# Optimization experiments

Measured on AMD Instinct MI355X. Metric: run time of the kernel, lower is better.

Reference implementation:

```python
import jax, jax.numpy as jnp
import numpy as np

EMBED_DIM = 1024
NUM_HEADS = 16
HEAD_DIM = EMBED_DIM // NUM_HEADS
B, L = 4, 2048


def setup_inputs() -> dict:
    key = jax.random.key(0)
    k1, k2, k3 = jax.random.split(key, 3)
    s = 1.0 / np.sqrt(EMBED_DIM)
    x = jax.random.normal(k1, (B, L, EMBED_DIM), dtype=jnp.float32)
    w_qkv = jax.random.normal(k2, (EMBED_DIM, 3 * EMBED_DIM), dtype=jnp.float32) * s
    b_qkv = jnp.zeros((3 * EMBED_DIM,), dtype=jnp.float32)
    w_out = jax.random.normal(k3, (EMBED_DIM, EMBED_DIM), dtype=jnp.float32) * s
    b_out = jnp.zeros((EMBED_DIM,), dtype=jnp.float32)
    return {"x": x, "w_qkv": w_qkv, "b_qkv": b_qkv, "w_out": w_out, "b_out": b_out}


def reference(x, w_qkv, b_qkv, w_out, b_out):
    Bb, Ll, _ = x.shape
    scale = HEAD_DIM ** -0.5
    qkv = x @ w_qkv + b_qkv                      # [B, L, 3E]
    qkv = qkv.reshape(Bb, Ll, 3, NUM_HEADS, HEAD_DIM)
    q, k, v = qkv[:, :, 0], qkv[:, :, 1], qkv[:, :, 2]   # [B, L, H, D]
    # scores: [B, H, L, L]
    scores = jnp.einsum("bqhd,bkhd->bhqk", q, k) * scale
    causal = jnp.tril(jnp.ones((Ll, Ll), dtype=bool))     # True = keep
    scores = jnp.where(causal, scores, jnp.float32(-1e9))
    attn_probs = jax.nn.softmax(scores, axis=-1)
    context = jnp.einsum("bhqk,bkhd->bqhd", attn_probs, v)
    context = context.reshape(Bb, Ll, EMBED_DIM)
    out = context @ w_out + b_out
    return (out, attn_probs)
```

## Files before the change

kernel.cpp:

```cpp
#include <hip/hip_runtime.h>


typedef __attribute__((ext_vector_type(8))) short short8;
typedef __attribute__((ext_vector_type(4))) float f32x4;

#define MFMA_BF16(a,b,c) __builtin_amdgcn_mfma_f32_16x16x32_bf16((a),(b),(c),0,0,0)

#define GLDS(gp, lp) __builtin_amdgcn_global_load_lds( \
    (const __attribute__((address_space(1))) unsigned int*)(gp), \
    (__attribute__((address_space(3))) unsigned int*)(lp), 16, 0, 0)

__device__ __forceinline__ unsigned short f2bf(float f) {
    union { float f; unsigned u; } v; v.f = f;
    return (unsigned short)((v.u + 0x7FFFu + ((v.u >> 16) & 1u)) >> 16);
}

#define QK_SCALE 0.18033688011112042f

__global__ __launch_bounds__(256) void k_cast(const float* __restrict__ src,
                                              unsigned short* __restrict__ dst, int n8) {
    int i = blockIdx.x * 256 + threadIdx.x;
    if (i >= n8) return;
    const float4* s = (const float4*)src + (size_t)i * 2;
    float4 a = s[0], b = s[1];
    short8 o;
    o[0] = f2bf(a.x); o[1] = f2bf(a.y); o[2] = f2bf(a.z); o[3] = f2bf(a.w);
    o[4] = f2bf(b.x); o[5] = f2bf(b.y); o[6] = f2bf(b.z); o[7] = f2bf(b.w);
    ((short8*)dst)[i] = o;
}

__global__ __launch_bounds__(256) void k_transpose_cast(const float* __restrict__ src,
                                                        unsigned short* __restrict__ dst,
                                                        int R, int C) {
    __shared__ unsigned short t[64][72];
    int c0 = blockIdx.x * 64, r0 = blockIdx.y * 64;
    int tid = threadIdx.x;
    int rl = tid >> 2, cs = (tid & 3) * 16;
    const float* sp = src + (size_t)(r0 + rl) * C + c0 + cs;
    #pragma unroll
    for (int j = 0; j < 16; j += 4) {
        float4 v = *(const float4*)(sp + j);
        t[rl][cs + j + 0] = f2bf(v.x);
        t[rl][cs + j + 1] = f2bf(v.y);
        t[rl][cs + j + 2] = f2bf(v.z);
        t[rl][cs + j + 3] = f2bf(v.w);
    }
    __syncthreads();
    int clq = tid >> 2, rs = (tid & 3) * 16;
    short8 o0, o1;
    #pragma unroll
    for (int j = 0; j < 8; ++j) o0[j] = (short)t[rs + j][clq];
    #pragma unroll
    for (int j = 0; j < 8; ++j) o1[j] = (short)t[rs + 8 + j][clq];
    unsigned short* dp = dst + (size_t)(c0 + clq) * R + r0 + rs;
    *(short8*)dp = o0;
    *(short8*)(dp + 8) = o1;
}

__global__ __launch_bounds__(256) void k_gemm_qkv(
    const unsigned short* __restrict__ A,
    const unsigned short* __restrict__ Bt,
    const float* __restrict__ bias,
    unsigned short* __restrict__ qb,
    unsigned short* __restrict__ kb,
    unsigned short* __restrict__ vb,
    float* __restrict__ probs)
{
    if (blockIdx.x >= 24) {
        const int c = blockIdx.x - 24;
        const int bh = blockIdx.y;
        const int tid = threadIdx.x;
        const f32x4 z = {0.f, 0.f, 0.f, 0.f};
        #pragma unroll
        for (int u = 0; u < 2; ++u) {
            const int tt = u == 0 ? c : 31 - c;
            const int col0 = (tt + 1) * 64;
            if (col0 >= 2048) continue;
            float* tp = probs + ((size_t)bh * 2048 + tt * 64) * 2048;
            for (int r = 0; r < 64; ++r) {
                float* rp = tp + (size_t)r * 2048;
                for (int cc = col0 + tid * 4; cc < 2048; cc += 1024)
                    __builtin_nontemporal_store(z, (f32x4*)&rp[cc]);
            }
        }
        return;
    }

    __shared__ unsigned short As[128 * 32];
    __shared__ unsigned short Bs[128 * 32];
    const int m0 = blockIdx.y * 128, n0 = blockIdx.x * 128;
    const int tid = threadIdx.x, w = tid >> 6, l = tid & 63;
    const int wm = w >> 1, wn = w & 1;
    const int g = l >> 4, cl = l & 15;
    const int srow = w * 16 + (l >> 2);
    const int soff = (l & 3) * 8;
    f32x4 acc[4][4] = {};

    for (int k0 = 0; k0 < 1024; k0 += 32) {
        __syncthreads();
        #pragma unroll
        for (int c = 0; c < 2; ++c) {
            GLDS(A  + (size_t)(m0 + c * 64 + srow) * 1024 + k0 + soff, &As[(c * 64 + w * 16) * 32]);
            GLDS(Bt + (size_t)(n0 + c * 64 + srow) * 1024 + k0 + soff, &Bs[(c * 64 + w * 16) * 32]);
        }
        __syncthreads();
        short8 af[4], bfr[4];
        #pragma unroll
        for (int i = 0; i < 4; ++i) af[i]  = *(const short8*)&As[(wm * 64 + i * 16 + cl) * 32 + g * 8];
        #pragma unroll
        for (int i = 0; i < 4; ++i) bfr[i] = *(const short8*)&Bs[(wn * 64 + i * 16 + cl) * 32 + g * 8];
        #pragma unroll
        for (int mi = 0; mi < 4; ++mi)
            #pragma unroll
            for (int ni = 0; ni < 4; ++ni)
                acc[mi][ni] = MFMA_BF16(af[mi], bfr[ni], acc[mi][ni]);
    }
    #pragma unroll
    for (int ni = 0; ni < 4; ++ni) {
        int col = n0 + wn * 64 + ni * 16 + cl;
        int which = col >> 10, h = (col >> 6) & 15, d = col & 63;
        unsigned short* dst = which == 0 ? qb : (which == 1 ? kb : vb);
        float bv = bias[col];
        float sc = (which == 0) ? QK_SCALE : 1.0f;
        #pragma unroll
        for (int mi = 0; mi < 4; ++mi) {
            #pragma unroll
            for (int i = 0; i < 4; ++i) {
                int row = m0 + wm * 64 + mi * 16 + g * 4 + i;
                int b = row >> 11, ll = row & 2047;
                dst[((size_t)(b * 16 + h) * 2048 + ll) * 64 + d] = f2bf((acc[mi][ni][i] + bv) * sc);
            }
        }
    }
}

__global__ __launch_bounds__(256) void k_gemm_out(
    const unsigned short* __restrict__ A,
    const unsigned short* __restrict__ Bt,
    const float* __restrict__ bias,
    float* __restrict__ out)
{
    __shared__ unsigned short As[128 * 32];
    __shared__ unsigned short Bs[128 * 32];
    const int m0 = blockIdx.y * 128, n0 = blockIdx.x * 128;
    const int tid = threadIdx.x, w = tid >> 6, l = tid & 63;
    const int wm = w >> 1, wn = w & 1;
    const int g = l >> 4, cl = l & 15;
    const int srow = w * 16 + (l >> 2);
    const int soff = (l & 3) * 8;
    f32x4 acc[4][4] = {};

    for (int k0 = 0; k0 < 1024; k0 += 32) {
        __syncthreads();
        #pragma unroll
        for (int c = 0; c < 2; ++c) {
            GLDS(A  + (size_t)(m0 + c * 64 + srow) * 1024 + k0 + soff, &As[(c * 64 + w * 16) * 32]);
            GLDS(Bt + (size_t)(n0 + c * 64 + srow) * 1024 + k0 + soff, &Bs[(c * 64 + w * 16) * 32]);
        }
        __syncthreads();
        short8 af[4], bfr[4];
        #pragma unroll
        for (int i = 0; i < 4; ++i) af[i]  = *(const short8*)&As[(wm * 64 + i * 16 + cl) * 32 + g * 8];
        #pragma unroll
        for (int i = 0; i < 4; ++i) bfr[i] = *(const short8*)&Bs[(wn * 64 + i * 16 + cl) * 32 + g * 8];
        #pragma unroll
        for (int mi = 0; mi < 4; ++mi)
            #pragma unroll
            for (int ni = 0; ni < 4; ++ni)
                acc[mi][ni] = MFMA_BF16(af[mi], bfr[ni], acc[mi][ni]);
    }
    #pragma unroll
    for (int ni = 0; ni < 4; ++ni) {
        int col = n0 + wn * 64 + ni * 16 + cl;
        float bv = bias[col];
        #pragma unroll
        for (int mi = 0; mi < 4; ++mi) {
            #pragma unroll
            for (int i = 0; i < 4; ++i) {
                int row = m0 + wm * 64 + mi * 16 + g * 4 + i;
                out[(size_t)row * 1024 + col] = acc[mi][ni][i] + bv;
            }
        }
    }
}

__device__ __forceinline__ void stage_qk(const unsigned short* gbase,
                                         unsigned short* lds, int w, int l) {
    const int lr = l >> 3;
    const int lc = (l & 7) ^ lr;
    #pragma unroll
    for (int c = 0; c < 2; ++c) {
        const int r0 = (w * 2 + c) * 8;
        GLDS(gbase + (size_t)(r0 + lr) * 64 + (lc << 3), lds + r0 * 64);
    }
}

__global__ __launch_bounds__(256, 4) void k_attn(
    const unsigned short* __restrict__ qb,
    const unsigned short* __restrict__ kb,
    const unsigned short* __restrict__ vb,
    float* __restrict__ probs,
    unsigned short* __restrict__ ctx)
{
    __shared__ unsigned short Ks[2][64 * 64];
    __shared__ unsigned short QV[64 * 64];
    __shared__ unsigned short Ps[4 * 16 * 64];

    const int lid = blockIdx.y * 32 + blockIdx.x;
    const int nl  = (lid & 7) * 256 + (lid >> 3);
    const int qt  = 31 - (nl & 31);
    const int bh  = nl >> 5;

    const int tid = threadIdx.x;
    const int w = tid >> 6, l = tid & 63;
    const int g = l >> 4, cl = l & 15;

    const unsigned short* Qg = qb + (size_t)bh * (2048 * 64);
    const unsigned short* Kg = kb + (size_t)bh * (2048 * 64);
    const unsigned short* Vg = vb + (size_t)bh * (2048 * 64);

    stage_qk(Qg + (size_t)qt * (64 * 64), QV, w, l);
    stage_qk(Kg, Ks[0], w, l);
    __syncthreads();

    const int qr = w * 16 + cl;
    short8 aq0 = *(const short8*)&QV[qr * 64 + ((g ^ (qr & 7)) << 3)];
    short8 aq1 = *(const short8*)&QV[qr * 64 + (((g + 4) ^ (qr & 7)) << 3)];

    f32x4 lpart = {0.f, 0.f, 0.f, 0.f};
    for (int kt = 0; kt <= qt; ++kt) {
        const unsigned short* K = Ks[kt & 1];
        if (kt < qt) {
            stage_qk(Kg + (size_t)(kt + 1) * (64 * 64), Ks[(kt & 1) ^ 1], w, l);
            #pragma unroll
            for (int kf = 0; kf < 4; ++kf) {
                int r = kf * 16 + cl;
                short8 b0 = *(const short8*)&K[r * 64 + ((g ^ (r & 7)) << 3)];
                short8 b1 = *(const short8*)&K[r * 64 + (((g + 4) ^ (r & 7)) << 3)];
                f32x4 acc = {0.f, 0.f, 0.f, 0.f};
                acc = MFMA_BF16(aq0, b0, acc);
                acc = MFMA_BF16(aq1, b1, acc);
                #pragma unroll
                for (int i = 0; i < 4; ++i)
                    lpart[i] += __builtin_amdgcn_exp2f(acc[i]);
            }
        } else {
            #pragma unroll
            for (int kf = 0; kf < 4; ++kf) {
                int r = kf * 16 + cl;
                short8 b0 = *(const short8*)&K[r * 64 + ((g ^ (r & 7)) << 3)];
                short8 b1 = *(const short8*)&K[r * 64 + (((g + 4) ^ (r & 7)) << 3)];
                f32x4 acc = {0.f, 0.f, 0.f, 0.f};
                acc = MFMA_BF16(aq0, b0, acc);
                acc = MFMA_BF16(aq1, b1, acc);
                #pragma unroll
                for (int i = 0; i < 4; ++i) {
                    float e = __builtin_amdgcn_exp2f(acc[i]);
                    lpart[i] += (r > w * 16 + g * 4 + i) ? 0.f : e;
                }
            }
        }
        __syncthreads();
    }

    f32x4 lr;
    #pragma unroll
    for (int i = 0; i < 4; ++i) {
        float s = lpart[i];
        s += __shfl_xor(s, 1);
        s += __shfl_xor(s, 2);
        s += __shfl_xor(s, 4);
        s += __shfl_xor(s, 8);
        lr[i] = -__log2f(s);
    }

    stage_qk(Kg, Ks[0], w, l);
    const int vkp = tid & 31;
    const int vd0 = (tid >> 5) * 8;
    short8 va  = *(const short8*)(Vg + (size_t)(2 * vkp) * 64 + vd0);
    short8 vb8 = *(const short8*)(Vg + (size_t)(2 * vkp + 1) * 64 + vd0);
    __syncthreads();

    f32x4 cacc[4] = {};
    unsigned int* Vt32 = (unsigned int*)QV;

    for (int kt = 0; kt <= qt; ++kt) {
        const unsigned short* K = Ks[kt & 1];
        const bool last = (kt == qt);
        if (!last) stage_qk(Kg + (size_t)(kt + 1) * (64 * 64), Ks[(kt & 1) ^ 1], w, l);

        #pragma unroll
        for (int j = 0; j < 8; ++j) {
            unsigned int pk = (unsigned int)(unsigned short)va[j]
                            | ((unsigned int)(unsigned short)vb8[j] << 16);
            Vt32[(vd0 + j) * 32 + (((vkp >> 2) ^ j) << 2) + (vkp & 3)] = pk;
        }
        if (!last) {
            va  = *(const short8*)(Vg + (size_t)((kt + 1) * 64 + 2 * vkp) * 64 + vd0);
            vb8 = *(const short8*)(Vg + (size_t)((kt + 1) * 64 + 2 * vkp + 1) * 64 + vd0);
        }

        size_t prow = ((size_t)bh * 2048 + qt * 64 + w * 16 + g * 4) * 2048 + kt * 64;
        #pragma unroll
        for (int kf = 0; kf < 4; ++kf) {
            int r = kf * 16 + cl;
            short8 b0 = *(const short8*)&K[r * 64 + ((g ^ (r & 7)) << 3)];
            short8 b1 = *(const short8*)&K[r * 64 + (((g + 4) ^ (r & 7)) << 3)];
            f32x4 acc = {0.f, 0.f, 0.f, 0.f};
            acc = MFMA_BF16(aq0, b0, acc);
            acc = MFMA_BF16(aq1, b1, acc);
            #pragma unroll
            for (int i = 0; i < 4; ++i) {
                float p = __builtin_amdgcn_exp2f(acc[i] + lr[i]);
                if (last && r > w * 16 + g * 4 + i) p = 0.f;
                __builtin_nontemporal_store(p, &probs[prow + (size_t)i * 2048 + kf * 16 + cl]);
                int rr = g * 4 + i;
                int scol = (((2 * kf + (cl >> 3)) ^ (rr & 7)) << 3) + (cl & 7);
                Ps[(w * 16 + rr) * 64 + scol] = f2bf(p);
            }
        }
        __syncthreads();

        #pragma unroll
        for (int kk = 0; kk < 2; ++kk) {
            short8 pa = *(const short8*)&Ps[(w * 16 + cl) * 64 + (((kk * 4 + g) ^ (cl & 7)) << 3)];
            #pragma unroll
            for (int df = 0; df < 4; ++df) {
                int vr = df * 16 + cl;
                short8 vf = *(const short8*)&QV[vr * 64 + (((kk * 4 + g) ^ (vr & 7)) << 3)];
                cacc[df] = MFMA_BF16(pa, vf, cacc[df]);
            }
        }
        __syncthreads();
    }

    {
        const int b = bh >> 4, h = bh & 15;
        #pragma unroll
        for (int df = 0; df < 4; ++df) {
            #pragma unroll
            for (int i = 0; i < 4; ++i) {
                int row = qt * 64 + w * 16 + g * 4 + i;
                ctx[((size_t)(b * 2048 + row)) * 1024 + h * 64 + df * 16 + cl] = f2bf(cacc[df][i]);
            }
        }
    }
}

extern "C" void kernel_launch(void* const* d_in, const int* in_sizes, int n_in,
                              void* d_out, int out_size, void* d_ws, size_t ws_size,
                              hipStream_t stream) {
    const float* x     = (const float*)d_in[0];
    const float* w_qkv = (const float*)d_in[1];
    const float* b_qkv = (const float*)d_in[2];
    const float* w_out = (const float*)d_in[3];
    const float* b_out = (const float*)d_in[4];

    float* out   = (float*)d_out;
    float* probs = out + (size_t)8192 * 1024;

    char* ws = (char*)d_ws;
    unsigned short* xb    = (unsigned short*)(ws);
    unsigned short* wqkvT = (unsigned short*)(ws + 16777216);
    unsigned short* woutT = (unsigned short*)(ws + 23068672);
    unsigned short* qb    = (unsigned short*)(ws + 25165824);
    unsigned short* kb    = (unsigned short*)(ws + 41943040);
    unsigned short* vb    = (unsigned short*)(ws + 58720256);
    unsigned short* ctx   = xb;

    k_cast<<<4096, 256, 0, stream>>>(x, xb, 1048576);
    k_transpose_cast<<<dim3(48, 16), 256, 0, stream>>>(w_qkv, wqkvT, 1024, 3072);
    k_transpose_cast<<<dim3(16, 16), 256, 0, stream>>>(w_out, woutT, 1024, 1024);
    k_gemm_qkv<<<dim3(40, 64), 256, 0, stream>>>(xb, wqkvT, b_qkv, qb, kb, vb, probs);
    k_attn<<<dim3(32, 64), 256, 0, stream>>>(qb, kb, vb, probs, ctx);
    k_gemm_out<<<dim3(8, 64), 256, 0, stream>>>(ctx, woutT, b_out, out);
}
```

Baseline: 386.5 us.

## Read K fragments directly from global and double-buffer V in LDS

Drops the LDS staging of K tiles: each wave now loads its K MFMA fragments straight from global memory in both the row-sum pass and the output pass. The freed LDS becomes a double buffer for transposed V, which lets the output loop use a single barrier per iteration instead of two. Shared-memory use drops, which may help occupancy. The cost is that every wave re-fetches the same K tile, so global/L1 traffic rises and the per-lane 16-byte loads are less well coalesced.

New measurement: 538.2 us. 1.39x slower.

```diff
diff --git a/kernel.cpp b/kernel.cpp
--- a/kernel.cpp
+++ b/kernel.cpp
@@ -184,8 +184,8 @@
     }
 }
 
-__device__ __forceinline__ void stage_qk(const unsigned short* gbase,
-                                         unsigned short* lds, int w, int l) {
+__device__ __forceinline__ void stage_q(const unsigned short* gbase,
+                                        unsigned short* lds, int w, int l) {
     const int lr = l >> 3;
     const int lc = (l & 7) ^ lr;
     #pragma unroll
@@ -202,8 +202,7 @@
     float* __restrict__ probs,
     unsigned short* __restrict__ ctx)
 {
-    __shared__ unsigned short Ks[2][64 * 64];
-    __shared__ unsigned short QV[64 * 64];
+    __shared__ unsigned short Vt[2][64 * 64];
     __shared__ unsigned short Ps[4 * 16 * 64];
 
     const int lid = blockIdx.y * 32 + blockIdx.x;
@@ -219,48 +218,50 @@
     const unsigned short* Kg = kb + (size_t)bh * (2048 * 64);
     const unsigned short* Vg = vb + (size_t)bh * (2048 * 64);
 
-    stage_qk(Qg + (size_t)qt * (64 * 64), QV, w, l);
-    stage_qk(Kg, Ks[0], w, l);
+    stage_q(Qg + (size_t)qt * (64 * 64), Vt[0], w, l);
     __syncthreads();
 
     const int qr = w * 16 + cl;
-    short8 aq0 = *(const short8*)&QV[qr * 64 + ((g ^ (qr & 7)) << 3)];
-    short8 aq1 = *(const short8*)&QV[qr * 64 + (((g + 4) ^ (qr & 7)) << 3)];
+    short8 aq0 = *(const short8*)&Vt[0][qr * 64 + ((g ^ (qr & 7)) << 3)];
+    short8 aq1 = *(const short8*)&Vt[0][qr * 64 + (((g + 4) ^ (qr & 7)) << 3)];
 
     f32x4 lpart = {0.f, 0.f, 0.f, 0.f};
-    for (int kt = 0; kt <= qt; ++kt) {
-        const unsigned short* K = Ks[kt & 1];
-        if (kt < qt) {
-            stage_qk(Kg + (size_t)(kt + 1) * (64 * 64), Ks[(kt & 1) ^ 1], w, l);
-            #pragma unroll
-            for (int kf = 0; kf < 4; ++kf) {
-                int r = kf * 16 + cl;
-                short8 b0 = *(const short8*)&K[r * 64 + ((g ^ (r & 7)) << 3)];
-                short8 b1 = *(const short8*)&K[r * 64 + (((g + 4) ^ (r & 7)) << 3)];
-                f32x4 acc = {0.f, 0.f, 0.f, 0.f};
-                acc = MFMA_BF16(aq0, b0, acc);
-                acc = MFMA_BF16(aq1, b1, acc);
-                #pragma unroll
-                for (int i = 0; i < 4; ++i)
-                    lpart[i] += __builtin_amdgcn_exp2f(acc[i]);
-            }
-        } else {
-            #pragma unroll
-            for (int kf = 0; kf < 4; ++kf) {
-                int r = kf * 16 + cl;
-                short8 b0 = *(const short8*)&K[r * 64 + ((g ^ (r & 7)) << 3)];
-                short8 b1 = *(const short8*)&K[r * 64 + (((g + 4) ^ (r & 7)) << 3)];
-                f32x4 acc = {0.f, 0.f, 0.f, 0.f};
-                acc = MFMA_BF16(aq0, b0, acc);
-                acc = MFMA_BF16(aq1, b1, acc);
-                #pragma unroll
-                for (int i = 0; i < 4; ++i) {
-                    float e = __builtin_amdgcn_exp2f(acc[i]);
-                    lpart[i] += (r > w * 16 + g * 4 + i) ? 0.f : e;
-                }
-            }
-        }
-        __syncthreads();
+    for (int kt = 0; kt < qt; ++kt) {
+        const unsigned short* Kt = Kg + (size_t)kt * (64 * 64);
+        short8 b0[4], b1[4];
+        #pragma unroll
+        for (int kf = 0; kf < 4; ++kf) {
+            const unsigned short* kr = Kt + (size_t)(kf * 16 + cl) * 64;
+            b0[kf] = *(const short8*)(kr + g * 8);
+            b1[kf] = *(const short8*)(kr + (g + 4) * 8);
+        }
+        #pragma unroll
+        for (int kf = 0; kf < 4; ++kf) {
+            f32x4 acc = {0.f, 0.f, 0.f, 0.f};
+            acc = MFMA_BF16(aq0, b0[kf], acc);
+            acc = MFMA_BF16(aq1, b1[kf], acc);
+            #pragma unroll
+            for (int i = 0; i < 4; ++i)
+                lpart[i] += __builtin_amdgcn_exp2f(acc[i]);
+        }
+    }
+    {
+        const unsigned short* Kt = Kg + (size_t)qt * (64 * 64);
+        #pragma unroll
+        for (int kf = 0; kf < 4; ++kf) {
+            int r = kf * 16 + cl;
+            const unsigned short* kr = Kt + (size_t)r * 64;
+            short8 b0 = *(const short8*)(kr + g * 8);
+            short8 b1 = *(const short8*)(kr + (g + 4) * 8);
+            f32x4 acc = {0.f, 0.f, 0.f, 0.f};
+            acc = MFMA_BF16(aq0, b0, acc);
+            acc = MFMA_BF16(aq1, b1, acc);
+            #pragma unroll
+            for (int i = 0; i < 4; ++i) {
+                float e = __builtin_amdgcn_exp2f(acc[i]);
+                lpart[i] += (r > w * 16 + g * 4 + i) ? 0.f : e;
+            }
+        }
     }
 
     f32x4 lr;
@@ -274,38 +275,40 @@
         lr[i] = -__log2f(s);
     }
 
-    stage_qk(Kg, Ks[0], w, l);
     const int vkp = tid & 31;
     const int vd0 = (tid >> 5) * 8;
     short8 va  = *(const short8*)(Vg + (size_t)(2 * vkp) * 64 + vd0);
     short8 vb8 = *(const short8*)(Vg + (size_t)(2 * vkp + 1) * 64 + vd0);
+
     __syncthreads();
 
     f32x4 cacc[4] = {};
-    unsigned int* Vt32 = (unsigned int*)QV;
 
     for (int kt = 0; kt <= qt; ++kt) {
-        const unsigned short* K = Ks[kt & 1];
+        const int cur = kt & 1;
         const bool last = (kt == qt);
-        if (!last) stage_qk(Kg + (size_t)(kt + 1) * (64 * 64), Ks[(kt & 1) ^ 1], w, l);
-
+
+        unsigned int* VtW = (unsigned int*)Vt[cur];
         #pragma unroll
         for (int j = 0; j < 8; ++j) {
             unsigned int pk = (unsigned int)(unsigned short)va[j]
                             | ((unsigned int)(unsigned short)vb8[j] << 16);
-            Vt32[(vd0 + j) * 32 + (((vkp >> 2) ^ j) << 2) + (vkp & 3)] = pk;
+            VtW[(vd0 + j) * 32 + (((vkp >> 2) ^ j) << 2) + (vkp & 3)] = pk;
         }
         if (!last) {
             va  = *(const short8*)(Vg + (size_t)((kt + 1) * 64 + 2 * vkp) * 64 + vd0);
             vb8 = *(const short8*)(Vg + (size_t)((kt + 1) * 64 + 2 * vkp + 1) * 64 + vd0);
         }
-
+        __syncthreads();
+
+        const unsigned short* Kt = Kg + (size_t)kt * (64 * 64);
         size_t prow = ((size_t)bh * 2048 + qt * 64 + w * 16 + g * 4) * 2048 + kt * 64;
         #pragma unroll
         for (int kf = 0; kf < 4; ++kf) {
             int r = kf * 16 + cl;
-            short8 b0 = *(const short8*)&K[r * 64 + ((g ^ (r & 7)) << 3)];
-            short8 b1 = *(const short8*)&K[r * 64 + (((g + 4) ^ (r & 7)) << 3)];
+            const unsigned short* kr = Kt + (size_t)r * 64;
+            short8 b0 = *(const short8*)(kr + g * 8);
+            short8 b1 = *(const short8*)(kr + (g + 4) * 8);
             f32x4 acc = {0.f, 0.f, 0.f, 0.f};
             acc = MFMA_BF16(aq0, b0, acc);
             acc = MFMA_BF16(aq1, b1, acc);
@@ -319,7 +322,6 @@
                 Ps[(w * 16 + rr) * 64 + scol] = f2bf(p);
             }
         }
-        __syncthreads();
 
         #pragma unroll
         for (int kk = 0; kk < 2; ++kk) {
@@ -327,11 +329,10 @@
             #pragma unroll
             for (int df = 0; df < 4; ++df) {
                 int vr = df * 16 + cl;
-                short8 vf = *(const short8*)&QV[vr * 64 + (((kk * 4 + g) ^ (vr & 7)) << 3)];
+                short8 vf = *(const short8*)&Vt[cur][vr * 64 + (((kk * 4 + g) ^ (vr & 7)) << 3)];
                 cacc[df] = MFMA_BF16(pa, vf, cacc[df]);
             }
         }
-        __syncthreads();
     }
 
     {
```
